# Kernel optimization log

Measured on AMD Instinct MI355X. Metric: run time of the kernel, lower is better.

## Reference

```python
import jax, jax.numpy as jnp
import numpy as np

N_NODES, N_EDGES = 50000, 25000
MAX_ARITY, MAX_DEG = 6, 8
NFEAT, NHID, NEMB, NHEADS = 128, 64, 128, 4
BATCH = 4096
ALPHA = 0.2
NEG = -1e9


def _attn_layer(hn_in, he_in, edge_list, node_list, Wn, We, a1, a2, concat):
    # hn_in [N,fin_n], he_in [E,fin_e]; edge_list [E,A] 1-based (0=pad); node_list [N,D] 1-based (0=pad)
    hn = hn_in @ Wn                      # [N,d]
    he = he_in @ We                      # [E,d]
    # --- stage 1: node -> edge attention ---
    emask = edge_list > 0                # [E,A]
    eidx = jnp.where(emask, edge_list - 1, 0)
    nd = hn[eidx]                        # [E,A,d]
    he_b = jnp.broadcast_to(he[:, None, :], nd.shape)
    s1 = jax.nn.leaky_relu(jnp.concatenate([he_b, nd], -1) @ a1, ALPHA)  # [E,A]
    att1 = jax.nn.softmax(jnp.where(emask, s1, NEG), axis=-1)
    edge_out = jnp.einsum('ea,ead->ed', att1, nd)  # [E,d]
    # --- stage 2: edge -> node attention ---
    nmask = node_list > 0                # [N,D]
    nidx = jnp.where(nmask, node_list - 1, 0)
    ed = edge_out[nidx]                  # [N,D,d]
    hn_b = jnp.broadcast_to(hn[:, None, :], ed.shape)
    s2 = jax.nn.leaky_relu(jnp.concatenate([hn_b, ed], -1) @ a2, ALPHA)  # [N,D]
    att2 = jax.nn.softmax(jnp.where(nmask, s2, NEG), axis=-1)
    node_out = jnp.einsum('nd,nde->ne', att2, ed)  # [N,d]
    if concat:
        node_out, edge_out = jax.nn.elu(node_out), jax.nn.elu(edge_out)
    return node_out, edge_out


def _forward(batch_inputs, edge_list, node_list, node_embs, edge_embs,
             Wn, We, a1, a2, Wn_o, We_o, a1_o, a2_o):
    # multi-head layers (vmap over head-stacked params)
    heads = jax.vmap(_attn_layer, in_axes=(None, None, None, None, 0, 0, 0, 0, None))
    hn, he = heads(node_embs, edge_embs, edge_list, node_list, Wn, We, a1, a2, True)
    H, N, d = hn.shape
    out_n = jnp.transpose(hn, (1, 0, 2)).reshape(N, H * d)          # concat heads
    out_e = jnp.transpose(he, (1, 0, 2)).reshape(he.shape[1], H * d)
    # dropout is identity in eval mode
    out_n, out_e = _attn_layer(out_n, out_e, edge_list, node_list, Wn_o, We_o, a1_o, a2_o, False)
    out_n, out_e = jax.nn.elu(out_n), jax.nn.elu(out_e)
    # --- build batch_outputs ---
    B, A1 = batch_inputs.shape
    nemb = out_e.shape[1]
    row0 = out_e[batch_inputs[:, 0] - 1]                            # [B,nemb] (col0 always >0)
    nids = batch_inputs[:, 1:] - 1
    nids = jnp.where(nids < 0, nids + out_n.shape[0], nids)         # torch-style negative wrap
    gathered = out_n[nids]                                          # [B,A1-1,nemb]
    last_nz = jnp.max(jnp.where(batch_inputs != 0, jnp.arange(A1)[None, :], -1), axis=1)  # right-1
    fill = (jnp.arange(1, A1)[None, :] <= last_nz[:, None])[:, :, None]
    rest = jnp.where(fill, gathered, jnp.ones((), gathered.dtype))
    return jnp.concatenate([row0[:, None, :], rest], axis=1)        # [B,A1,nemb]


def setup_inputs() -> dict:
    key = jax.random.key(0)
    ks = jax.random.split(key, 12)
    f32 = jnp.float32
    node_embs = jax.random.normal(ks[0], (N_NODES, NFEAT), f32) * 0.02
    edge_embs = jax.random.normal(ks[1], (N_EDGES, NFEAT), f32) * 0.02
    # ragged incidence with 0-padding (1-based ids)
    el = jax.random.randint(ks[2], (N_EDGES, MAX_ARITY), 1, N_NODES + 1)
    earity = jax.random.randint(ks[3], (N_EDGES, 1), 2, MAX_ARITY + 1)
    edge_list = jnp.where(jnp.arange(MAX_ARITY)[None, :] < earity, el, 0)
    nl = jax.random.randint(ks[4], (N_NODES, MAX_DEG), 1, N_EDGES + 1)
    ndeg = jax.random.randint(ks[5], (N_NODES, 1), 1, MAX_DEG + 1)
    node_list = jnp.where(jnp.arange(MAX_DEG)[None, :] < ndeg, nl, 0)
    # batch: col0 = edge id, cols 1.. = node ids, right-padded with 0
    bi_e = jax.random.randint(ks[6], (BATCH, 1), 1, N_EDGES + 1)
    bi_n = jax.random.randint(ks[7], (BATCH, MAX_ARITY), 1, N_NODES + 1)
    barity = jax.random.randint(ks[8], (BATCH, 1), 2, MAX_ARITY + 1)
    bi_n = jnp.where(jnp.arange(MAX_ARITY)[None, :] < barity, bi_n, 0)
    batch_inputs = jnp.concatenate([bi_e, bi_n], axis=1)
    def glorot(k, shape):
        lim = np.sqrt(6.0 / (shape[-2] + shape[-1]))
        return jax.random.uniform(k, shape, f32, -lim, lim)
    return {
        'batch_inputs': batch_inputs, 'edge_list': edge_list, 'node_list': node_list,
        'node_embs': node_embs, 'edge_embs': edge_embs,
        'Wn': glorot(ks[9], (NHEADS, NFEAT, NHID)),
        'We': glorot(ks[10], (NHEADS, NFEAT, NHID)),
        'a1': jax.random.normal(ks[11], (NHEADS, 2 * NHID), f32) * 0.1,
        'a2': jax.random.normal(jax.random.fold_in(key, 20), (NHEADS, 2 * NHID), f32) * 0.1,
        'Wn_o': glorot(jax.random.fold_in(key, 21), (NHID * NHEADS, NEMB)),
        'We_o': glorot(jax.random.fold_in(key, 22), (NHID * NHEADS, NEMB)),
        'a1_o': jax.random.normal(jax.random.fold_in(key, 23), (2 * NEMB,), f32) * 0.1,
        'a2_o': jax.random.normal(jax.random.fold_in(key, 24), (2 * NEMB,), f32) * 0.1,
    }


def reference(batch_inputs, edge_list, node_list, node_embs, edge_embs,
              Wn, We, a1, a2, Wn_o, We_o, a1_o, a2_o):
    return _forward(batch_inputs, edge_list, node_list, node_embs, edge_embs,
                    Wn, We, a1, a2, Wn_o, We_o, a1_o, a2_o)
```

## Files before the change

kernel.cpp:

```cpp
#include <hip/hip_runtime.h>
#include <math.h>

#define N_NODES 50000
#define N_EDGES 25000
#define MAX_ARITY 6
#define MAX_DEG 8
#define NFEAT 128
#define NHID 64
#define NEMB 128
#define NHEADS 4
#define BATCH 4096

#define MT_N 3128

typedef __bf16 bf16x8 __attribute__((ext_vector_type(8)));
typedef __bf16 bf16x4 __attribute__((ext_vector_type(4)));
typedef float f32x4 __attribute__((ext_vector_type(4)));
typedef float f32x2 __attribute__((ext_vector_type(2)));

__device__ __forceinline__ float wave_sum(float v) {
#pragma unroll
    for (int off = 1; off < 64; off <<= 1) v += __shfl_xor(v, off);
    return v;
}
__device__ __forceinline__ float group32_sum(float v) {
#pragma unroll
    for (int off = 1; off < 32; off <<= 1) v += __shfl_xor(v, off);
    return v;
}
__device__ __forceinline__ float group16_sum(float v) {
#pragma unroll
    for (int off = 1; off < 16; off <<= 1) v += __shfl_xor(v, off);
    return v;
}
__device__ __forceinline__ float group8_sum(float v) {
#pragma unroll
    for (int off = 1; off < 8; off <<= 1) v += __shfl_xor(v, off);
    return v;
}
__device__ __forceinline__ float lrelu(float x) { return x >= 0.f ? x : 0.2f * x; }
__device__ __forceinline__ float eluf(float x) { return x > 0.f ? x : expm1f(x); }

__device__ __forceinline__ int2 pack_fp8x8(const float* v) {
    int w0 = __builtin_amdgcn_cvt_pk_fp8_f32(v[0], v[1], 0, 0);
    w0 = __builtin_amdgcn_cvt_pk_fp8_f32(v[2], v[3], w0, 1);
    int w1 = __builtin_amdgcn_cvt_pk_fp8_f32(v[4], v[5], 0, 0);
    w1 = __builtin_amdgcn_cvt_pk_fp8_f32(v[6], v[7], w1, 1);
    int2 o;
    o.x = w0;
    o.y = w1;
    return o;
}
__device__ __forceinline__ void unpack_fp8x8(int2 w, float* v) {
    f32x2 a = __builtin_amdgcn_cvt_pk_f32_fp8(w.x, false);
    f32x2 b = __builtin_amdgcn_cvt_pk_f32_fp8(w.x, true);
    f32x2 c = __builtin_amdgcn_cvt_pk_f32_fp8(w.y, false);
    f32x2 d = __builtin_amdgcn_cvt_pk_f32_fp8(w.y, true);
    v[0] = a[0]; v[1] = a[1]; v[2] = b[0]; v[3] = b[1];
    v[4] = c[0]; v[5] = c[1]; v[6] = d[0]; v[7] = d[1];
}
__device__ __forceinline__ unsigned char fp8_of(float x) {
    return (unsigned char)(__builtin_amdgcn_cvt_pk_fp8_f32(x, x, 0, 0) & 0xff);
}

#define PREP_REPACK_BLKS 3128
#define PREP_BCONV1_BLKS 16
#define PREP_BCONV2_BLKS 16
#define PREP_WVEC1_BLKS 2
#define PREP_WVEC2_BLKS 1
#define PREP_C1_BLKS 6250
#define PREP_TOTAL_BLKS (PREP_REPACK_BLKS + PREP_BCONV1_BLKS + PREP_BCONV2_BLKS + \
                         PREP_WVEC1_BLKS + PREP_WVEC2_BLKS + PREP_C1_BLKS)

__global__ __launch_bounds__(256) void prep_kernel(
    const float* __restrict__ node_embs, const float* __restrict__ edge_embs,
    const float* __restrict__ Wn, const float* __restrict__ We, const float* __restrict__ a1,
    const float* __restrict__ Wn_o, const float* __restrict__ We_o,
    const float* __restrict__ a1_o, __bf16* __restrict__ A1n, __bf16* __restrict__ B1n,
    __bf16* __restrict__ B2n, float* __restrict__ wc1, float* __restrict__ wc2,
    float* __restrict__ c1) {
    int blk = blockIdx.x;
    if (blk < PREP_REPACK_BLKS) {
        int t = blk * 256 + threadIdx.x;
        int lane = t & 63;
        int kt = (t >> 6) & 3;
        int mt = t >> 8;
        int row = mt * 16 + (lane & 15);
        int ks = kt * 32 + (lane >> 4) * 8;
        float v[8];
        if (row < N_NODES) {
            float4 p0 = *reinterpret_cast<const float4*>(node_embs + (size_t)row * 128 + ks);
            float4 p1 = *reinterpret_cast<const float4*>(node_embs + (size_t)row * 128 + ks + 4);
            v[0] = p0.x; v[1] = p0.y; v[2] = p0.z; v[3] = p0.w;
            v[4] = p1.x; v[5] = p1.y; v[6] = p1.z; v[7] = p1.w;
        } else {
#pragma unroll
            for (int j = 0; j < 8; ++j) v[j] = 0.f;
        }
        bf16x8 o;
#pragma unroll
        for (int j = 0; j < 8; ++j) o[j] = (__bf16)v[j];
        reinterpret_cast<bf16x8*>(A1n)[t] = o;
        return;
    }
    blk -= PREP_REPACK_BLKS;
    if (blk < PREP_BCONV1_BLKS) {
        int t = blk * 256 + threadIdx.x;
        int lane = t & 63;
        int nt = (t >> 6) & 15;
        int kt = t >> 10;
        int k0 = kt * 32 + (lane >> 4) * 8;
        int h = nt >> 2;
        int nl = (nt & 3) * 16 + (lane & 15);
        bf16x8 o;
#pragma unroll
        for (int j = 0; j < 8; ++j) o[j] = (__bf16)Wn[(h * NFEAT + k0 + j) * NHID + nl];
        reinterpret_cast<bf16x8*>(B1n)[t] = o;
        return;
    }
    blk -= PREP_BCONV1_BLKS;
    if (blk < PREP_BCONV2_BLKS) {
        int t = blk * 256 + threadIdx.x;
        int lane = t & 63;
        int nt = (t >> 6) & 7;
        int kt = t >> 9;
        int k0 = kt * 32 + (lane >> 4) * 8;
        int n = nt * 16 + (lane & 15);
        bf16x8 o;
#pragma unroll
        for (int j = 0; j < 8; ++j) o[j] = (__bf16)Wn_o[(size_t)(k0 + j) * 128 + n];
        reinterpret_cast<bf16x8*>(B2n)[t] = o;
        return;
    }
    blk -= PREP_BCONV2_BLKS;
    if (blk < PREP_WVEC1_BLKS) {
        int t = blk * 256 + threadIdx.x;
        int h = t >> 7, k = t & 127;
        float s = 0.f;
        for (int j = 0; j < 64; ++j) s += We[(h * NFEAT + k) * NHID + j] * a1[h * 128 + j];
        wc1[t] = s;
        return;
    }
    blk -= PREP_WVEC1_BLKS;
    if (blk < PREP_WVEC2_BLKS) {
        int t = threadIdx.x;
        float s = 0.f;
        for (int j = 0; j < 128; ++j) s += We_o[(size_t)t * 128 + j] * a1_o[j];
        wc2[t] = s;
        return;
    }
    blk -= PREP_WVEC2_BLKS;
    {
        int r = blk * 4 + (threadIdx.x >> 6);
        int lane = threadIdx.x & 63;
        if (r >= N_EDGES) return;
        float x0 = edge_embs[(size_t)r * 128 + lane];
        float x1 = edge_embs[(size_t)r * 128 + 64 + lane];
#pragma unroll
        for (int h = 0; h < 4; ++h) {
            float s = wave_sum(x0 * wc1[h * 128 + lane] + x1 * wc1[h * 128 + 64 + lane]);
            if (lane == 0) c1[r * 4 + h] = s;
        }
    }
}

template <int KT, int BNF, int DOTMODE, int NDOTV, int MPW, bool C8>
__global__ __launch_bounds__(256) void mgemm_kernel(
    const __bf16* __restrict__ A, const __bf16* __restrict__ B, void* __restrict__ Cout, int M,
    int N, int NTB, const float* __restrict__ vA, int offA, float* __restrict__ outA,
    const float* __restrict__ vB, int offB, float* __restrict__ outB) {
    const int w = threadIdx.x >> 6, l = threadIdx.x & 63;
    const int mtb = blockIdx.y * (4 * MPW) + w * MPW;
    const int nbf = blockIdx.x * BNF;
    f32x4 acc[MPW][BNF];
#pragma unroll
    for (int i = 0; i < MPW; ++i)
#pragma unroll
        for (int j = 0; j < BNF; ++j) acc[i][j] = (f32x4){0.f, 0.f, 0.f, 0.f};
    const bf16x8* Ap = reinterpret_cast<const bf16x8*>(A) + (size_t)mtb * KT * 64 + l;
    const bf16x8* Bp = reinterpret_cast<const bf16x8*>(B) + l;
#pragma unroll
    for (int kt = 0; kt < KT; ++kt) {
        bf16x8 a[MPW];
#pragma unroll
        for (int mi = 0; mi < MPW; ++mi) a[mi] = Ap[((size_t)mi * KT + kt) * 64];
#pragma unroll
        for (int nj = 0; nj < BNF; ++nj) {
            bf16x8 b = Bp[((size_t)kt * NTB + nbf + nj) * 64];
#pragma unroll
            for (int mi = 0; mi < MPW; ++mi)
                acc[mi][nj] = __builtin_amdgcn_mfma_f32_16x16x32_bf16(a[mi], b, acc[mi][nj], 0, 0, 0);
        }
    }
    const int rq = (l >> 4) * 4;
    const int cl = l & 15;
#pragma unroll
    for (int mi = 0; mi < MPW; ++mi) {
        int mbase = (mtb + mi) * 16 + rq;
#pragma unroll
        for (int q = 0; q < 4; ++q) {
            int m = mbase + q;
            if (m < M) {
#pragma unroll
                for (int nj = 0; nj < BNF; ++nj) {
                    if (C8) {
                        ((unsigned char*)Cout)[(size_t)m * N + (nbf + nj) * 16 + cl] =
                            fp8_of(acc[mi][nj][q]);
                    } else {
                        ((__bf16*)Cout)[(size_t)m * N + (nbf + nj) * 16 + cl] =
                            (__bf16)acc[mi][nj][q];
                    }
                }
            }
        }
    }
    if (DOTMODE) {
        float va[BNF], vb[BNF];
        const int vbase = (DOTMODE == 1) ? (nbf >> 2) * 128 : 0;
#pragma unroll
        for (int nj = 0; nj < BNF; ++nj) {
            int col = (DOTMODE == 1) ? ((nbf + nj) & 3) * 16 + cl : (nbf + nj) * 16 + cl;
            va[nj] = vA[vbase + offA + col];
            if (NDOTV >= 2) vb[nj] = vB[vbase + offB + col];
        }
        const int outStride = (DOTMODE == 1) ? 4 : 1;
        const int outOff = (DOTMODE == 1) ? (nbf >> 2) : 0;
#pragma unroll
        for (int mi = 0; mi < MPW; ++mi) {
#pragma unroll
            for (int q = 0; q < 4; ++q) {
                float pA = 0.f, pB = 0.f;
#pragma unroll
                for (int nj = 0; nj < BNF; ++nj) {
                    pA += acc[mi][nj][q] * va[nj];
                    if (NDOTV >= 2) pB += acc[mi][nj][q] * vb[nj];
                }
                pA = group16_sum(pA);
                if (NDOTV >= 2) pB = group16_sum(pB);
                int m = (mtb + mi) * 16 + rq + q;
                if (cl == 0 && m < M) {
                    outA[(size_t)m * outStride + outOff] = pA;
                    if (NDOTV >= 2) outB[(size_t)m * outStride + outOff] = pB;
                }
            }
        }
    }
}

__global__ __launch_bounds__(256) void attn64e_kernel(
    const int* __restrict__ nbr, const unsigned char* __restrict__ feat,
    const float* __restrict__ sdot, const float* __restrict__ ndot,
    const float* __restrict__ a2v, const float* __restrict__ wc2,
    unsigned char* __restrict__ eo1, float* __restrict__ f1, float* __restrict__ c2, int rows) {
    const int lane = threadIdx.x & 63;
    const int half = lane >> 5, lp = lane & 31;
    const int r = (blockIdx.x * 4 + (threadIdx.x >> 6)) * 2 + half;
    if (r >= rows) return;
    const int h = lp >> 3;
    int id[MAX_ARITY];
    bool val[MAX_ARITY];
#pragma unroll
    for (int a = 0; a < MAX_ARITY; ++a) {
        int v = nbr[r * MAX_ARITY + a];
        val[a] = v > 0;
        id[a] = val[a] ? (v - 1) : 0;
    }
    int2 f8[MAX_ARITY];
    float nd[MAX_ARITY];
#pragma unroll
    for (int a = 0; a < MAX_ARITY; ++a) {
        f8[a] = *reinterpret_cast<const int2*>(feat + (size_t)id[a] * 256 + lp * 8);
        nd[a] = ndot[(size_t)id[a] * 4 + h];
    }
    const float c = sdot[r * 4 + h];
    float wgt[MAX_ARITY];
    float smax = -1e30f;
#pragma unroll
    for (int a = 0; a < MAX_ARITY; ++a) {
        float s = val[a] ? lrelu(c + nd[a]) : -3e30f;
        wgt[a] = s;
        if (val[a]) smax = fmaxf(smax, s);
    }
    float denom = 0.f;
#pragma unroll
    for (int a = 0; a < MAX_ARITY; ++a) {
        float ex = val[a] ? expf(wgt[a] - smax) : 0.f;
        wgt[a] = ex;
        denom += ex;
    }
    float inv = 1.f / denom;
    float acc[8] = {0.f, 0.f, 0.f, 0.f, 0.f, 0.f, 0.f, 0.f};
#pragma unroll
    for (int a = 0; a < MAX_ARITY; ++a) {
        float fv[8];
        unpack_fp8x8(f8[a], fv);
#pragma unroll
        for (int j = 0; j < 8; ++j) acc[j] = fmaf(wgt[a], fv[j], acc[j]);
    }
#pragma unroll
    for (int j = 0; j < 8; ++j) acc[j] *= inv;
    *reinterpret_cast<int2*>(eo1 + (size_t)r * 256 + lp * 8) = pack_fp8x8(acc);
    float p = 0.f;
#pragma unroll
    for (int j = 0; j < 8; ++j) p += acc[j] * a2v[h * 128 + 64 + (lp & 7) * 8 + j];
    p = group8_sum(p);
    if ((lp & 7) == 0) f1[r * 4 + h] = p;
    float p2 = 0.f;
#pragma unroll
    for (int j = 0; j < 8; ++j) p2 += eluf(acc[j]) * wc2[lp * 8 + j];
    p2 = group32_sum(p2);
    if (lp == 0) c2[r] = p2;
}

__global__ __launch_bounds__(256) void attn64n_kernel(const int* __restrict__ nbr,
                                                      const unsigned char* __restrict__ feat,
                                                      const float* __restrict__ sdot,
                                                      const float* __restrict__ ndot,
                                                      __bf16* __restrict__ Afrag, int rows,
                                                      int rowsPad) {
    const int lane = threadIdx.x & 63;
    const int half = lane >> 5, lp = lane & 31;
    const int r = (blockIdx.x * 4 + (threadIdx.x >> 6)) * 2 + half;
    if (r >= rowsPad) return;
    const int rr = r & 15, mt = r >> 4;
    const int kt = lp >> 2, g = lp & 3;
    __bf16* dptr = Afrag + ((((size_t)mt * 8 + kt) * 64 + g * 16 + rr) << 3);
    if (r >= rows) {
        bf16x8 z;
#pragma unroll
        for (int j = 0; j < 8; ++j) z[j] = (__bf16)0.f;
        *reinterpret_cast<bf16x8*>(dptr) = z;
        return;
    }
    const int h = lp >> 3;
    int id[MAX_DEG];
    bool val[MAX_DEG];
#pragma unroll
    for (int a = 0; a < MAX_DEG; ++a) {
        int v = nbr[r * MAX_DEG + a];
        val[a] = v > 0;
        id[a] = val[a] ? (v - 1) : 0;
    }
    int2 f8[MAX_DEG];
    float nd[MAX_DEG];
#pragma unroll
    for (int a = 0; a < MAX_DEG; ++a) {
        f8[a] = *reinterpret_cast<const int2*>(feat + (size_t)id[a] * 256 + lp * 8);
        nd[a] = ndot[(size_t)id[a] * 4 + h];
    }
    const float c = sdot[r * 4 + h];
    float wgt[MAX_DEG];
    float smax = -1e30f;
#pragma unroll
    for (int a = 0; a < MAX_DEG; ++a) {
        float s = val[a] ? lrelu(c + nd[a]) : -3e30f;
        wgt[a] = s;
        if (val[a]) smax = fmaxf(smax, s);
    }
    float denom = 0.f;
#pragma unroll
    for (int a = 0; a < MAX_DEG; ++a) {
        float ex = val[a] ? expf(wgt[a] - smax) : 0.f;
        wgt[a] = ex;
        denom += ex;
    }
    float inv = 1.f / denom;
    float acc[8] = {0.f, 0.f, 0.f, 0.f, 0.f, 0.f, 0.f, 0.f};
#pragma unroll
    for (int a = 0; a < MAX_DEG; ++a) {
        float fv[8];
        unpack_fp8x8(f8[a], fv);
#pragma unroll
        for (int j = 0; j < 8; ++j) acc[j] = fmaf(wgt[a], fv[j], acc[j]);
    }
    bf16x8 o;
#pragma unroll
    for (int j = 0; j < 8; ++j) o[j] = (__bf16)eluf(acc[j] * inv);
    *reinterpret_cast<bf16x8*>(dptr) = o;
}

template <int NNBR, bool DOT>
__global__ __launch_bounds__(256) void attn128_kernel(const int* __restrict__ nbr,
                                                      const __bf16* __restrict__ feat,
                                                      const float* __restrict__ sdot,
                                                      const float* __restrict__ ndot,
                                                      const float* __restrict__ fvec,
                                                      __bf16* __restrict__ outF,
                                                      float* __restrict__ outDot, int rows) {
    const int lane = threadIdx.x & 63;
    const int qt = lane >> 4, lq = lane & 15;
    const int r = (blockIdx.x * 4 + (threadIdx.x >> 6)) * 4 + qt;
    if (r >= rows) return;
    int id[NNBR];
    bool val[NNBR];
#pragma unroll
    for (int a = 0; a < NNBR; ++a) {
        int v = nbr[r * NNBR + a];
        val[a] = v > 0;
        id[a] = val[a] ? (v - 1) : 0;
    }
    bf16x8 f8[NNBR];
    float nd[NNBR];
#pragma unroll
    for (int a = 0; a < NNBR; ++a) {
        f8[a] = *reinterpret_cast<const bf16x8*>(feat + (size_t)id[a] * 128 + lq * 8);
        nd[a] = ndot[id[a]];
    }
    const float c = sdot[r];
    float wgt[NNBR];
    float smax = -1e30f;
#pragma unroll
    for (int a = 0; a < NNBR; ++a) {
        float s = val[a] ? lrelu(c + nd[a]) : -3e30f;
        wgt[a] = s;
        if (val[a]) smax = fmaxf(smax, s);
    }
    float denom = 0.f;
#pragma unroll
    for (int a = 0; a < NNBR; ++a) {
        float ex = val[a] ? expf(wgt[a] - smax) : 0.f;
        wgt[a] = ex;
        denom += ex;
    }
    float inv = 1.f / denom;
    float acc[8] = {0.f, 0.f, 0.f, 0.f, 0.f, 0.f, 0.f, 0.f};
#pragma unroll
    for (int a = 0; a < NNBR; ++a)
#pragma unroll
        for (int j = 0; j < 8; ++j) acc[j] = fmaf(wgt[a], (float)f8[a][j], acc[j]);
    bf16x8 o;
#pragma unroll
    for (int j = 0; j < 8; ++j) {
        acc[j] *= inv;
        o[j] = (__bf16)acc[j];
    }
    *reinterpret_cast<bf16x8*>(outF + (size_t)r * 128 + lq * 8) = o;
    if (DOT) {
        float p = 0.f;
#pragma unroll
        for (int j = 0; j < 8; ++j) p += acc[j] * fvec[128 + lq * 8 + j];
        p = group16_sum(p);
        if (lq == 0) outDot[r] = p;
    }
}

__global__ __launch_bounds__(256) void batch_kernel(const int* __restrict__ bi,
                                                    const __bf16* __restrict__ eo2,
                                                    const __bf16* __restrict__ no2,
                                                    float* __restrict__ out) {
    const int lane = threadIdx.x & 63;
    const int half = lane >> 5, lp = lane & 31;
    const int gw = (blockIdx.x * 4 + (threadIdx.x >> 6)) * 2 + half;
    if (gw >= BATCH * 7) return;
    int b = gw / 7, s = gw % 7;
    int last_nz = -1;
#pragma unroll
    for (int j = 0; j < 7; ++j)
        if (bi[b * 7 + j] != 0) last_nz = j;
    float4 v;
    if (s == 0) {
        int e = bi[b * 7] - 1;
        bf16x4 t = *reinterpret_cast<const bf16x4*>(eo2 + (size_t)e * 128 + lp * 4);
        v = make_float4(eluf((float)t[0]), eluf((float)t[1]), eluf((float)t[2]),
                        eluf((float)t[3]));
    } else if (s <= last_nz) {
        int nid = bi[b * 7 + s] - 1;
        if (nid < 0) nid += N_NODES;
        bf16x4 t = *reinterpret_cast<const bf16x4*>(no2 + (size_t)nid * 128 + lp * 4);
        v = make_float4(eluf((float)t[0]), eluf((float)t[1]), eluf((float)t[2]),
                        eluf((float)t[3]));
    } else {
        v = make_float4(1.f, 1.f, 1.f, 1.f);
    }
    *reinterpret_cast<float4*>(out + (size_t)b * 896 + s * 128 + lp * 4) = v;
}

extern "C" void kernel_launch(void* const* d_in, const int* in_sizes, int n_in,
                              void* d_out, int out_size, void* d_ws, size_t ws_size,
                              hipStream_t stream) {
    const int* batch_inputs = (const int*)d_in[0];
    const int* edge_list = (const int*)d_in[1];
    const int* node_list = (const int*)d_in[2];
    const float* node_embs = (const float*)d_in[3];
    const float* edge_embs = (const float*)d_in[4];
    const float* Wn = (const float*)d_in[5];
    const float* We = (const float*)d_in[6];
    const float* a1 = (const float*)d_in[7];
    const float* a2 = (const float*)d_in[8];
    const float* Wn_o = (const float*)d_in[9];
    const float* We_o = (const float*)d_in[10];
    const float* a1_o = (const float*)d_in[11];
    const float* a2_o = (const float*)d_in[12];
    float* out = (float*)d_out;
    char* ws = (char*)d_ws;

    __bf16* A1n = (__bf16*)(ws);
    __bf16* B1n = (__bf16*)(ws + 12812288);
    __bf16* B2n = (__bf16*)(ws + 12877824);
    float* wc1 = (float*)(ws + 12943360);
    float* wc2 = (float*)(ws + 12945408);
    float* c1 = (float*)(ws + 12946432);
    float* d1 = (float*)(ws + 13346432);
    float* g1v = (float*)(ws + 14146432);
    float* f1 = (float*)(ws + 14946432);
    float* c2 = (float*)(ws + 15346432);
    float* d2 = (float*)(ws + 15446432);
    float* g2v = (float*)(ws + 15646432);
    float* f2 = (float*)(ws + 15846432);
    unsigned char* hn1 = (unsigned char*)(ws + 16000000);
    __bf16* A2n = (__bf16*)(ws + 28800000);
    __bf16* hn2 = (__bf16*)(ws + 54424576);
    unsigned char* eo1 = (unsigned char*)(ws + 67224576);
    __bf16* no2 = (__bf16*)(ws + 67224576);
    __bf16* eo2 = (__bf16*)(ws + 80024576);

    prep_kernel<<<PREP_TOTAL_BLKS, 256, 0, stream>>>(node_embs, edge_embs, Wn, We, a1, Wn_o,
                                                     We_o, a1_o, A1n, B1n, B2n, wc1, wc2, c1);

    {
        dim3 g(4, MT_N / 8);
        mgemm_kernel<4, 4, 1, 2, 2, true><<<g, 256, 0, stream>>>(
            A1n, B1n, hn1, N_NODES, 256, 16, a1, 64, d1, a2, 0, g1v);
    }
    attn64e_kernel<<<(N_EDGES / 2 + 3) / 4, 256, 0, stream>>>(edge_list, hn1, c1, d1, a2, wc2,
                                                              eo1, f1, c2, N_EDGES);
    attn64n_kernel<<<(MT_N * 16 / 2 + 3) / 4, 256, 0, stream>>>(node_list, eo1, g1v, f1, A2n,
                                                                N_NODES, MT_N * 16);
    {
        dim3 g(1, MT_N / 4);
        mgemm_kernel<8, 8, 2, 2, 1, false><<<g, 256, 0, stream>>>(
            A2n, B2n, hn2, N_NODES, 128, 8, a1_o, 128, d2, a2_o, 0, g2v);
    }
    attn128_kernel<MAX_ARITY, true><<<(N_EDGES / 4 + 3) / 4, 256, 0, stream>>>(
        edge_list, hn2, c2, d2, a2_o, eo2, f2, N_EDGES);
    attn128_kernel<MAX_DEG, false><<<(N_NODES / 4 + 3) / 4, 256, 0, stream>>>(
        node_list, eo2, g2v, f2, nullptr, no2, nullptr, N_NODES);
    batch_kernel<<<(BATCH * 7 / 2 + 3) / 4, 256, 0, stream>>>(batch_inputs, eo2, no2, out);
}
```

Measured before the change: 206.0 us.

## Fuse node attention with second GEMM via LDS and read fp32 embeddings directly

The separate bf16 repack of node_embs is removed: the first GEMM now loads fp32 rows and converts them to bf16 in registers. The node-side attention of layer 1 is fused with the layer-2 projection GEMM. Each block computes 64 attended rows into shared memory and then runs MFMA on them, so the A2n fragment buffer no longer makes a round trip through global memory. The cost is uncoalesced fp32 A loads in the first GEMM, about 33KB of LDS per block, and a serialized gather-then-GEMM phase in each block, which may lower occupancy.

```diff
diff --git a/kernel.cpp b/kernel.cpp
--- a/kernel.cpp
+++ b/kernel.cpp
@@ -63,47 +63,21 @@
     return (unsigned char)(__builtin_amdgcn_cvt_pk_fp8_f32(x, x, 0, 0) & 0xff);
 }
 
-#define PREP_REPACK_BLKS 3128
 #define PREP_BCONV1_BLKS 16
 #define PREP_BCONV2_BLKS 16
 #define PREP_WVEC1_BLKS 2
 #define PREP_WVEC2_BLKS 1
 #define PREP_C1_BLKS 6250
-#define PREP_TOTAL_BLKS (PREP_REPACK_BLKS + PREP_BCONV1_BLKS + PREP_BCONV2_BLKS + \
+#define PREP_TOTAL_BLKS (PREP_BCONV1_BLKS + PREP_BCONV2_BLKS + \
                          PREP_WVEC1_BLKS + PREP_WVEC2_BLKS + PREP_C1_BLKS)
 
 __global__ __launch_bounds__(256) void prep_kernel(
-    const float* __restrict__ node_embs, const float* __restrict__ edge_embs,
-    const float* __restrict__ Wn, const float* __restrict__ We, const float* __restrict__ a1,
-    const float* __restrict__ Wn_o, const float* __restrict__ We_o,
-    const float* __restrict__ a1_o, __bf16* __restrict__ A1n, __bf16* __restrict__ B1n,
+    const float* __restrict__ edge_embs, const float* __restrict__ Wn,
+    const float* __restrict__ We, const float* __restrict__ a1, const float* __restrict__ Wn_o,
+    const float* __restrict__ We_o, const float* __restrict__ a1_o, __bf16* __restrict__ B1n,
     __bf16* __restrict__ B2n, float* __restrict__ wc1, float* __restrict__ wc2,
     float* __restrict__ c1) {
     int blk = blockIdx.x;
-    if (blk < PREP_REPACK_BLKS) {
-        int t = blk * 256 + threadIdx.x;
-        int lane = t & 63;
-        int kt = (t >> 6) & 3;
-        int mt = t >> 8;
-        int row = mt * 16 + (lane & 15);
-        int ks = kt * 32 + (lane >> 4) * 8;
-        float v[8];
-        if (row < N_NODES) {
-            float4 p0 = *reinterpret_cast<const float4*>(node_embs + (size_t)row * 128 + ks);
-            float4 p1 = *reinterpret_cast<const float4*>(node_embs + (size_t)row * 128 + ks + 4);
-            v[0] = p0.x; v[1] = p0.y; v[2] = p0.z; v[3] = p0.w;
-            v[4] = p1.x; v[5] = p1.y; v[6] = p1.z; v[7] = p1.w;
-        } else {
-#pragma unroll
-            for (int j = 0; j < 8; ++j) v[j] = 0.f;
-        }
-        bf16x8 o;
-#pragma unroll
-        for (int j = 0; j < 8; ++j) o[j] = (__bf16)v[j];
-        reinterpret_cast<bf16x8*>(A1n)[t] = o;
-        return;
-    }
-    blk -= PREP_REPACK_BLKS;
     if (blk < PREP_BCONV1_BLKS) {
         int t = blk * 256 + threadIdx.x;
         int lane = t & 63;
@@ -164,84 +138,79 @@
     }
 }
 
-template <int KT, int BNF, int DOTMODE, int NDOTV, int MPW, bool C8>
-__global__ __launch_bounds__(256) void mgemm_kernel(
-    const __bf16* __restrict__ A, const __bf16* __restrict__ B, void* __restrict__ Cout, int M,
-    int N, int NTB, const float* __restrict__ vA, int offA, float* __restrict__ outA,
-    const float* __restrict__ vB, int offB, float* __restrict__ outB) {
+__global__ __launch_bounds__(256) void mgemm1_kernel(
+    const float* __restrict__ Af32, const __bf16* __restrict__ B,
+    unsigned char* __restrict__ C, const float* __restrict__ a1v,
+    const float* __restrict__ a2v, float* __restrict__ d1, float* __restrict__ g1v) {
     const int w = threadIdx.x >> 6, l = threadIdx.x & 63;
-    const int mtb = blockIdx.y * (4 * MPW) + w * MPW;
-    const int nbf = blockIdx.x * BNF;
-    f32x4 acc[MPW][BNF];
-#pragma unroll
-    for (int i = 0; i < MPW; ++i)
-#pragma unroll
-        for (int j = 0; j < BNF; ++j) acc[i][j] = (f32x4){0.f, 0.f, 0.f, 0.f};
-    const bf16x8* Ap = reinterpret_cast<const bf16x8*>(A) + (size_t)mtb * KT * 64 + l;
+    const int mtb = blockIdx.y * 8 + w * 2;
+    const int nbf = blockIdx.x * 4;
+    const int lr = l & 15, lk = (l >> 4) * 8;
+    f32x4 acc[2][4];
+#pragma unroll
+    for (int i = 0; i < 2; ++i)
+#pragma unroll
+        for (int j = 0; j < 4; ++j) acc[i][j] = (f32x4){0.f, 0.f, 0.f, 0.f};
     const bf16x8* Bp = reinterpret_cast<const bf16x8*>(B) + l;
 #pragma unroll
-    for (int kt = 0; kt < KT; ++kt) {
-        bf16x8 a[MPW];
-#pragma unroll
-        for (int mi = 0; mi < MPW; ++mi) a[mi] = Ap[((size_t)mi * KT + kt) * 64];
-#pragma unroll
-        for (int nj = 0; nj < BNF; ++nj) {
-            bf16x8 b = Bp[((size_t)kt * NTB + nbf + nj) * 64];
-#pragma unroll
-            for (int mi = 0; mi < MPW; ++mi)
+    for (int kt = 0; kt < 4; ++kt) {
+        bf16x8 a[2];
+#pragma unroll
+        for (int mi = 0; mi < 2; ++mi) {
+            int row = (mtb + mi) * 16 + lr;
+            int ks = kt * 32 + lk;
+            float v[8];
+            if (row < N_NODES) {
+                float4 p0 = *reinterpret_cast<const float4*>(Af32 + (size_t)row * 128 + ks);
+                float4 p1 = *reinterpret_cast<const float4*>(Af32 + (size_t)row * 128 + ks + 4);
+                v[0] = p0.x; v[1] = p0.y; v[2] = p0.z; v[3] = p0.w;
+                v[4] = p1.x; v[5] = p1.y; v[6] = p1.z; v[7] = p1.w;
+            } else {
+#pragma unroll
+                for (int j = 0; j < 8; ++j) v[j] = 0.f;
+            }
+#pragma unroll
+            for (int j = 0; j < 8; ++j) a[mi][j] = (__bf16)v[j];
+        }
+#pragma unroll
+        for (int nj = 0; nj < 4; ++nj) {
+            bf16x8 b = Bp[((size_t)kt * 16 + nbf + nj) * 64];
+#pragma unroll
+            for (int mi = 0; mi < 2; ++mi)
                 acc[mi][nj] = __builtin_amdgcn_mfma_f32_16x16x32_bf16(a[mi], b, acc[mi][nj], 0, 0, 0);
         }
     }
     const int rq = (l >> 4) * 4;
     const int cl = l & 15;
-#pragma unroll
-    for (int mi = 0; mi < MPW; ++mi) {
-        int mbase = (mtb + mi) * 16 + rq;
+    const int h = nbf >> 2;
+    float va[4], vb[4];
+#pragma unroll
+    for (int nj = 0; nj < 4; ++nj) {
+        int col = ((nbf + nj) & 3) * 16 + cl;
+        va[nj] = a1v[h * 128 + 64 + col];
+        vb[nj] = a2v[h * 128 + col];
+    }
+#pragma unroll
+    for (int mi = 0; mi < 2; ++mi) {
 #pragma unroll
         for (int q = 0; q < 4; ++q) {
-            int m = mbase + q;
-            if (m < M) {
-#pragma unroll
-                for (int nj = 0; nj < BNF; ++nj) {
-                    if (C8) {
-                        ((unsigned char*)Cout)[(size_t)m * N + (nbf + nj) * 16 + cl] =
-                            fp8_of(acc[mi][nj][q]);
-                    } else {
-                        ((__bf16*)Cout)[(size_t)m * N + (nbf + nj) * 16 + cl] =
-                            (__bf16)acc[mi][nj][q];
-                    }
-                }
+            int m = (mtb + mi) * 16 + rq + q;
+            float pA = 0.f, pB = 0.f;
+#pragma unroll
+            for (int nj = 0; nj < 4; ++nj) {
+                pA += acc[mi][nj][q] * va[nj];
+                pB += acc[mi][nj][q] * vb[nj];
             }
-        }
-    }
-    if (DOTMODE) {
-        float va[BNF], vb[BNF];
-        const int vbase = (DOTMODE == 1) ? (nbf >> 2) * 128 : 0;
-#pragma unroll
-        for (int nj = 0; nj < BNF; ++nj) {
-            int col = (DOTMODE == 1) ? ((nbf + nj) & 3) * 16 + cl : (nbf + nj) * 16 + cl;
-            va[nj] = vA[vbase + offA + col];
-            if (NDOTV >= 2) vb[nj] = vB[vbase + offB + col];
-        }
-        const int outStride = (DOTMODE == 1) ? 4 : 1;
-        const int outOff = (DOTMODE == 1) ? (nbf >> 2) : 0;
-#pragma unroll
-        for (int mi = 0; mi < MPW; ++mi) {
-#pragma unroll
-            for (int q = 0; q < 4; ++q) {
-                float pA = 0.f, pB = 0.f;
-#pragma unroll
-                for (int nj = 0; nj < BNF; ++nj) {
-                    pA += acc[mi][nj][q] * va[nj];
-                    if (NDOTV >= 2) pB += acc[mi][nj][q] * vb[nj];
-                }
-                pA = group16_sum(pA);
-                if (NDOTV >= 2) pB = group16_sum(pB);
-                int m = (mtb + mi) * 16 + rq + q;
-                if (cl == 0 && m < M) {
-                    outA[(size_t)m * outStride + outOff] = pA;
-                    if (NDOTV >= 2) outB[(size_t)m * outStride + outOff] = pB;
-                }
+            if (m < N_NODES) {
+#pragma unroll
+                for (int nj = 0; nj < 4; ++nj)
+                    C[(size_t)m * 256 + (nbf + nj) * 16 + cl] = fp8_of(acc[mi][nj][q]);
+            }
+            pA = group16_sum(pA);
+            pB = group16_sum(pB);
+            if (cl == 0 && m < N_NODES) {
+                d1[m * 4 + h] = pA;
+                g1v[m * 4 + h] = pB;
             }
         }
     }
@@ -312,71 +281,120 @@
     if (lp == 0) c2[r] = p2;
 }
 
-__global__ __launch_bounds__(256) void attn64n_kernel(const int* __restrict__ nbr,
-                                                      const unsigned char* __restrict__ feat,
-                                                      const float* __restrict__ sdot,
-                                                      const float* __restrict__ ndot,
-                                                      __bf16* __restrict__ Afrag, int rows,
-                                                      int rowsPad) {
-    const int lane = threadIdx.x & 63;
+#define LDSW 260
+
+__global__ __launch_bounds__(256) void fuse2_kernel(
+    const int* __restrict__ nbr, const unsigned char* __restrict__ feat,
+    const float* __restrict__ sdot, const float* __restrict__ ndot,
+    const __bf16* __restrict__ B, __bf16* __restrict__ hn2, const float* __restrict__ a1o,
+    const float* __restrict__ a2o, float* __restrict__ d2, float* __restrict__ g2v) {
+    __shared__ __bf16 Alds[64 * LDSW];
+    const int w = threadIdx.x >> 6, lane = threadIdx.x & 63;
     const int half = lane >> 5, lp = lane & 31;
-    const int r = (blockIdx.x * 4 + (threadIdx.x >> 6)) * 2 + half;
-    if (r >= rowsPad) return;
-    const int rr = r & 15, mt = r >> 4;
-    const int kt = lp >> 2, g = lp & 3;
-    __bf16* dptr = Afrag + ((((size_t)mt * 8 + kt) * 64 + g * 16 + rr) << 3);
-    if (r >= rows) {
-        bf16x8 z;
-#pragma unroll
-        for (int j = 0; j < 8; ++j) z[j] = (__bf16)0.f;
-        *reinterpret_cast<bf16x8*>(dptr) = z;
-        return;
-    }
     const int h = lp >> 3;
-    int id[MAX_DEG];
-    bool val[MAX_DEG];
-#pragma unroll
-    for (int a = 0; a < MAX_DEG; ++a) {
-        int v = nbr[r * MAX_DEG + a];
-        val[a] = v > 0;
-        id[a] = val[a] ? (v - 1) : 0;
-    }
-    int2 f8[MAX_DEG];
-    float nd[MAX_DEG];
-#pragma unroll
-    for (int a = 0; a < MAX_DEG; ++a) {
-        f8[a] = *reinterpret_cast<const int2*>(feat + (size_t)id[a] * 256 + lp * 8);
-        nd[a] = ndot[(size_t)id[a] * 4 + h];
-    }
-    const float c = sdot[r * 4 + h];
-    float wgt[MAX_DEG];
-    float smax = -1e30f;
-#pragma unroll
-    for (int a = 0; a < MAX_DEG; ++a) {
-        float s = val[a] ? lrelu(c + nd[a]) : -3e30f;
-        wgt[a] = s;
-        if (val[a]) smax = fmaxf(smax, s);
-    }
-    float denom = 0.f;
-#pragma unroll
-    for (int a = 0; a < MAX_DEG; ++a) {
-        float ex = val[a] ? expf(wgt[a] - smax) : 0.f;
-        wgt[a] = ex;
-        denom += ex;
-    }
-    float inv = 1.f / denom;
-    float acc[8] = {0.f, 0.f, 0.f, 0.f, 0.f, 0.f, 0.f, 0.f};
-#pragma unroll
-    for (int a = 0; a < MAX_DEG; ++a) {
-        float fv[8];
-        unpack_fp8x8(f8[a], fv);
-#pragma unroll
-        for (int j = 0; j < 8; ++j) acc[j] = fmaf(wgt[a], fv[j], acc[j]);
-    }
-    bf16x8 o;
-#pragma unroll
-    for (int j = 0; j < 8; ++j) o[j] = (__bf16)eluf(acc[j] * inv);
-    *reinterpret_cast<bf16x8*>(dptr) = o;
+#pragma unroll
+    for (int p = 0; p < 8; ++p) {
+        const int rl = w * 16 + p * 2 + half;
+        const int r = blockIdx.x * 64 + rl;
+        __bf16* dptr = &Alds[rl * LDSW + lp * 8];
+        if (r >= N_NODES) {
+            bf16x8 z;
+#pragma unroll
+            for (int j = 0; j < 8; ++j) z[j] = (__bf16)0.f;
+            *reinterpret_cast<bf16x8*>(dptr) = z;
+            continue;
+        }
+        int id[MAX_DEG];
+        bool val[MAX_DEG];
+#pragma unroll
+        for (int a = 0; a < MAX_DEG; ++a) {
+            int v = nbr[r * MAX_DEG + a];
+            val[a] = v > 0;
+            id[a] = val[a] ? (v - 1) : 0;
+        }
+        int2 f8[MAX_DEG];
+        float nd[MAX_DEG];
+#pragma unroll
+        for (int a = 0; a < MAX_DEG; ++a) {
+            f8[a] = *reinterpret_cast<const int2*>(feat + (size_t)id[a] * 256 + lp * 8);
+            nd[a] = ndot[(size_t)id[a] * 4 + h];
+        }
+        const float c = sdot[r * 4 + h];
+        float wgt[MAX_DEG];
+        float smax = -1e30f;
+#pragma unroll
+        for (int a = 0; a < MAX_DEG; ++a) {
+            float s = val[a] ? lrelu(c + nd[a]) : -3e30f;
+            wgt[a] = s;
+            if (val[a]) smax = fmaxf(smax, s);
+        }
+        float denom = 0.f;
+#pragma unroll
+        for (int a = 0; a < MAX_DEG; ++a) {
+            float ex = val[a] ? expf(wgt[a] - smax) : 0.f;
+            wgt[a] = ex;
+            denom += ex;
+        }
+        float inv = 1.f / denom;
+        float acc[8] = {0.f, 0.f, 0.f, 0.f, 0.f, 0.f, 0.f, 0.f};
+#pragma unroll
+        for (int a = 0; a < MAX_DEG; ++a) {
+            float fv[8];
+            unpack_fp8x8(f8[a], fv);
+#pragma unroll
+            for (int j = 0; j < 8; ++j) acc[j] = fmaf(wgt[a], fv[j], acc[j]);
+        }
+        bf16x8 o;
+#pragma unroll
+        for (int j = 0; j < 8; ++j) o[j] = (__bf16)eluf(acc[j] * inv);
+        *reinterpret_cast<bf16x8*>(dptr) = o;
+    }
+    __syncthreads();
+    const int lr = lane & 15, lkq = lane >> 4;
+    f32x4 acc[8];
+#pragma unroll
+    for (int j = 0; j < 8; ++j) acc[j] = (f32x4){0.f, 0.f, 0.f, 0.f};
+    const bf16x8* Bp = reinterpret_cast<const bf16x8*>(B) + lane;
+#pragma unroll
+    for (int kt = 0; kt < 8; ++kt) {
+        bf16x8 a = *reinterpret_cast<const bf16x8*>(
+            &Alds[(w * 16 + lr) * LDSW + kt * 32 + lkq * 8]);
+#pragma unroll
+        for (int nj = 0; nj < 8; ++nj) {
+            bf16x8 b = Bp[((size_t)kt * 8 + nj) * 64];
+            acc[nj] = __builtin_amdgcn_mfma_f32_16x16x32_bf16(a, b, acc[nj], 0, 0, 0);
+        }
+    }
+    const int rq = lkq * 4;
+    const int cl = lane & 15;
+    const int gm0 = blockIdx.x * 64 + w * 16 + rq;
+    float va[8], vb[8];
+#pragma unroll
+    for (int nj = 0; nj < 8; ++nj) {
+        va[nj] = a1o[128 + nj * 16 + cl];
+        vb[nj] = a2o[nj * 16 + cl];
+    }
+#pragma unroll
+    for (int q = 0; q < 4; ++q) {
+        int m = gm0 + q;
+        float pA = 0.f, pB = 0.f;
+#pragma unroll
+        for (int nj = 0; nj < 8; ++nj) {
+            pA += acc[nj][q] * va[nj];
+            pB += acc[nj][q] * vb[nj];
+        }
+        if (m < N_NODES) {
+#pragma unroll
+            for (int nj = 0; nj < 8; ++nj)
+                hn2[(size_t)m * 128 + nj * 16 + cl] = (__bf16)acc[nj][q];
+        }
+        pA = group16_sum(pA);
+        pB = group16_sum(pB);
+        if (cl == 0 && m < N_NODES) {
+            d2[m] = pA;
+            g2v[m] = pB;
+        }
+    }
 }
 
 template <int NNBR, bool DOT>
@@ -494,43 +512,35 @@
     float* out = (float*)d_out;
     char* ws = (char*)d_ws;
 
-    __bf16* A1n = (__bf16*)(ws);
-    __bf16* B1n = (__bf16*)(ws + 12812288);
-    __bf16* B2n = (__bf16*)(ws + 12877824);
-    float* wc1 = (float*)(ws + 12943360);
-    float* wc2 = (float*)(ws + 12945408);
-    float* c1 = (float*)(ws + 12946432);
-    float* d1 = (float*)(ws + 13346432);
-    float* g1v = (float*)(ws + 14146432);
-    float* f1 = (float*)(ws + 14946432);
-    float* c2 = (float*)(ws + 15346432);
-    float* d2 = (float*)(ws + 15446432);
-    float* g2v = (float*)(ws + 15646432);
-    float* f2 = (float*)(ws + 15846432);
-    unsigned char* hn1 = (unsigned char*)(ws + 16000000);
-    __bf16* A2n = (__bf16*)(ws + 28800000);
-    __bf16* hn2 = (__bf16*)(ws + 54424576);
-    unsigned char* eo1 = (unsigned char*)(ws + 67224576);
-    __bf16* no2 = (__bf16*)(ws + 67224576);
-    __bf16* eo2 = (__bf16*)(ws + 80024576);
-
-    prep_kernel<<<PREP_TOTAL_BLKS, 256, 0, stream>>>(node_embs, edge_embs, Wn, We, a1, Wn_o,
-                                                     We_o, a1_o, A1n, B1n, B2n, wc1, wc2, c1);
+    __bf16* B1n = (__bf16*)(ws);
+    __bf16* B2n = (__bf16*)(ws + 65536);
+    float* wc1 = (float*)(ws + 131072);
+    float* wc2 = (float*)(ws + 133120);
+    float* c1 = (float*)(ws + 134144);
+    float* d1 = (float*)(ws + 534144);
+    float* g1v = (float*)(ws + 1334144);
+    float* f1 = (float*)(ws + 2134144);
+    float* c2 = (float*)(ws + 2534144);
+    float* d2 = (float*)(ws + 2634144);
+    float* g2v = (float*)(ws + 2834144);
+    float* f2 = (float*)(ws + 3034144);
+    unsigned char* hn1 = (unsigned char*)(ws + 3134144);
+    __bf16* hn2 = (__bf16*)(ws + 15934144);
+    unsigned char* eo1 = (unsigned char*)(ws + 28734144);
+    __bf16* eo2 = (__bf16*)(ws + 35134144);
+    __bf16* no2 = (__bf16*)(ws + 41534144);
+
+    prep_kernel<<<PREP_TOTAL_BLKS, 256, 0, stream>>>(edge_embs, Wn, We, a1, Wn_o, We_o, a1_o,
+                                                     B1n, B2n, wc1, wc2, c1);
 
     {
         dim3 g(4, MT_N / 8);
-        mgemm_kernel<4, 4, 1, 2, 2, true><<<g, 256, 0, stream>>>(
-            A1n, B1n, hn1, N_NODES, 256, 16, a1, 64, d1, a2, 0, g1v);
+        mgemm1_kernel<<<g, 256, 0, stream>>>(node_embs, B1n, hn1, a1, a2, d1, g1v);
     }
     attn64e_kernel<<<(N_EDGES / 2 + 3) / 4, 256, 0, stream>>>(edge_list, hn1, c1, d1, a2, wc2,
                                                               eo1, f1, c2, N_EDGES);
-    attn64n_kernel<<<(MT_N * 16 / 2 + 3) / 4, 256, 0, stream>>>(node_list, eo1, g1v, f1, A2n,
-                                                                N_NODES, MT_N * 16);
-    {
-        dim3 g(1, MT_N / 4);
-        mgemm_kernel<8, 8, 2, 2, 1, false><<<g, 256, 0, stream>>>(
-            A2n, B2n, hn2, N_NODES, 128, 8, a1_o, 128, d2, a2_o, 0, g2v);
-    }
+    fuse2_kernel<<<MT_N / 4, 256, 0, stream>>>(node_list, eo1, g1v, f1, B2n, hn2, a1_o, a2_o,
+                                               d2, g2v);
     attn128_kernel<MAX_ARITY, true><<<(N_EDGES / 4 + 3) / 4, 256, 0, stream>>>(
         edge_list, hn2, c2, d2, a2_o, eo2, f2, N_EDGES);
     attn128_kernel<MAX_DEG, false><<<(N_NODES / 4 + 3) / 4, 256, 0, stream>>>(
```

Result: slower. 218.5 us (+6.1%).
